# Kernel optimization log

Measured on AMD Instinct MI355X. Metric: run time of the kernel, lower is better.

The kernel has to match this reference:

```python
import jax, jax.numpy as jnp
import numpy as np

K = 16                 # k nearest neighbors
POS_LO, POS_HI = 0, 3  # position_slice
INF = jnp.float32(1e30)


def setup_inputs() -> dict:
    key = jax.random.key(0)
    k1, k2, k3 = jax.random.split(key, 3)
    B, N, F = 16, 2048, 128
    nodes = jax.random.normal(k1, (B, N, F), dtype=jnp.float32)
    T = jax.random.randint(k2, (B,), 0, 1024)
    taus = jax.random.randint(k3, (B,), 0, 1024)
    return {"nodes": nodes, "T": T, "taus": taus, "B": B}


def reference(nodes, T, taus, B):
    # Faithful, vectorized version of the per-batch causal KNN edge builder.
    # Original: for each batch b, sinks = pos[b, T[b]:T[b]+taus[b]],
    # sources = pos[b, :T[b]+taus[b]]; knn(source, sink, k) returns
    # (sink_local_idx, source_idx); keep edges where sink_local > source;
    # assemble COO adjacency (b, sink_local, source) with weight 1.
    # Here we return the equivalent DENSE [B, N, N] adjacency.
    pos = nodes[:, :, POS_LO:POS_HI]              # [B, N, d]
    N = pos.shape[1]
    i_idx = jnp.arange(N)                         # local sink index grid
    # global index of sink i in batch b is T[b] + i
    sink_gidx = jnp.clip(T[:, None] + i_idx[None, :], 0, N - 1)   # [B, N]
    sink_pos = jnp.take_along_axis(pos, sink_gidx[..., None], axis=1)  # [B, N, d]
    sink_valid = i_idx[None, :] < taus[:, None]                    # [B, N]
    src_valid = i_idx[None, :] < (T + taus)[:, None]               # [B, N]
    # squared distances sink->source: [B, N_sink, N_src]
    d2 = jnp.sum((sink_pos[:, :, None, :] - pos[:, None, :, :]) ** 2, axis=-1)
    d2 = jnp.where(src_valid[:, None, :], d2, INF)
    neg_vals, nbr = jax.lax.top_k(-d2, K)          # k smallest distances, [B, N, K]
    nbr_valid = neg_vals > -INF                    # source actually existed
    causal = i_idx[None, :, None] > nbr            # edge[0] > edge[1] mask (local sink idx)
    valid = sink_valid[:, :, None] & nbr_valid & causal
    adj = jnp.zeros((B, N, N), dtype=jnp.float32)
    b_idx = jnp.arange(B)[:, None, None]
    adj = adj.at[b_idx, i_idx[None, :, None], nbr].add(
        jnp.where(valid, jnp.float32(1.0), jnp.float32(0.0)))
    return adj
```

## Files before the change

kernel.cpp:

```cpp
#include <hip/hip_runtime.h>

#define NN 2048
#define FF 128
#define KK 16
#define INF_KEY 0xFFFFFFFFFFFFFFFFull

typedef float f32x4 __attribute__((ext_vector_type(4)));

__device__ __forceinline__ unsigned wave_min_u32(unsigned x) {
    int v = (int)x, t;
    t = __builtin_amdgcn_update_dpp(v, v, 0x111, 0xf, 0xf, false);
    v = ((unsigned)t < (unsigned)v) ? t : v;
    t = __builtin_amdgcn_update_dpp(v, v, 0x112, 0xf, 0xf, false);
    v = ((unsigned)t < (unsigned)v) ? t : v;
    t = __builtin_amdgcn_update_dpp(v, v, 0x114, 0xf, 0xf, false);
    v = ((unsigned)t < (unsigned)v) ? t : v;
    t = __builtin_amdgcn_update_dpp(v, v, 0x118, 0xf, 0xf, false);
    v = ((unsigned)t < (unsigned)v) ? t : v;
    t = __builtin_amdgcn_update_dpp(v, v, 0x142, 0xf, 0xf, false);
    v = ((unsigned)t < (unsigned)v) ? t : v;
    t = __builtin_amdgcn_update_dpp(v, v, 0x143, 0xf, 0xf, false);
    v = ((unsigned)t < (unsigned)v) ? t : v;
    return (unsigned)__builtin_amdgcn_readlane(v, 63);
}

__global__ __launch_bounds__(256) void pack_xyz(
    const float* __restrict__ nodes, f32x4* __restrict__ out, int total)
{
    const int t = blockIdx.x * 256 + threadIdx.x;
    if (t < total) {
        const float* p = nodes + (size_t)t * FF;
        out[t] = (f32x4){p[0], p[1], p[2], 0.f};
    }
}

template<bool PACKED>
__device__ __forceinline__ f32x4 load_xyz(const float* __restrict__ base, int idx) {
    if constexpr (PACKED) {
        return ((const f32x4*)base)[idx];
    } else {
        const float* p = base + (size_t)idx * FF;
        return (f32x4){p[0], p[1], p[2], 0.f};
    }
}

template<bool PACKED>
__global__ __launch_bounds__(256, 8) void knn_scatter(
    const float* __restrict__ xyz,
    const int*   __restrict__ T_arr,
    const int*   __restrict__ tau_arr,
    float*       __restrict__ adj)
{
    const int b    = blockIdx.x;
    const int i0   = blockIdx.y << 2;
    const int tid  = threadIdx.x;
    const int wave = tid >> 6;
    const int lane = tid & 63;

    const int tau = tau_arr[b];
    if (i0 >= tau) return;

    const int i = i0 + wave;
    if (i >= tau) return;

    const int T = T_arr[b];
    const int M = T + tau;
    const float* base = PACKED ? xyz + (size_t)b * NN * 4
                               : xyz + (size_t)b * NN * FF;
    float* row = adj + ((size_t)b * NN + i) * NN;

    const int g = T + i;
    const f32x4 sp = load_xyz<PACKED>(base, g);
    const float sxv = sp.x, syv = sp.y, szv = sp.z;

    unsigned long long q0 = INF_KEY, q1 = INF_KEY, q2 = INF_KEY, q3 = INF_KEY;
    const int S = (M + 63) >> 6;
    #pragma unroll 4
    for (int s = 0; s < S; ++s) {
        const int j = lane + (s << 6);
        if (j < M) {
            const f32x4 v = load_xyz<PACKED>(base, j);
            float dx = __fsub_rn(sxv, v.x);
            float dy = __fsub_rn(syv, v.y);
            float dz = __fsub_rn(szv, v.z);
            float d2 = __fadd_rn(__fadd_rn(__fmul_rn(dx, dx), __fmul_rn(dy, dy)),
                                 __fmul_rn(dz, dz));
            unsigned long long key =
                ((unsigned long long)__float_as_uint(d2) << 32) | (unsigned)(j + 1);
            if (key < q3) {
                q3 = key;
                unsigned long long t;
                if (q3 < q2) { t = q2; q2 = q3; q3 = t; }
                if (q2 < q1) { t = q1; q1 = q2; q2 = t; }
                if (q1 < q0) { t = q0; q0 = q1; q1 = t; }
            }
        }
    }

    unsigned long long lastpop = 0;
    for (int k = 0; k < KK; ++k) {
        const unsigned hd = (unsigned)(q0 >> 32);
        const unsigned m  = wave_min_u32(hd);
        if (m == 0xFFFFFFFFu) break;

        const unsigned long long mask = __ballot(hd == m);
        unsigned jwin;
        if (__popcll(mask) == 1) {
            const int w = __builtin_ctzll(mask);
            jwin = (unsigned)__builtin_amdgcn_readlane((int)(unsigned)q0, w);
        } else {
            unsigned jc = (hd == m) ? (unsigned)q0 : 0xFFFFFFFFu;
            jwin = wave_min_u32(jc);
        }
        const int j = (int)jwin - 1;

        if (lane == 0 && j < i)
            row[j] = 1.0f;

        if (hd == m && (unsigned)q0 == jwin) {
            lastpop = ((unsigned long long)m << 32) | jwin;
            q0 = q1; q1 = q2; q2 = q3; q3 = INF_KEY;
            if (q0 == INF_KEY) {
                unsigned long long best = INF_KEY;
                for (int s2 = 0; s2 < S; ++s2) {
                    const int jj = lane + (s2 << 6);
                    if (jj < M) {
                        const f32x4 v = load_xyz<PACKED>(base, jj);
                        float dx = __fsub_rn(sxv, v.x);
                        float dy = __fsub_rn(syv, v.y);
                        float dz = __fsub_rn(szv, v.z);
                        float d2 = __fadd_rn(
                            __fadd_rn(__fmul_rn(dx, dx), __fmul_rn(dy, dy)),
                            __fmul_rn(dz, dz));
                        unsigned long long kk =
                            ((unsigned long long)__float_as_uint(d2) << 32)
                            | (unsigned)(jj + 1);
                        if (kk > lastpop && kk < best) best = kk;
                    }
                }
                q0 = best;
            }
        }
    }
}

extern "C" void kernel_launch(void* const* d_in, const int* in_sizes, int n_in,
                              void* d_out, int out_size, void* d_ws, size_t ws_size,
                              hipStream_t stream) {
    const float* nodes = (const float*)d_in[0];
    const int*   T     = (const int*)d_in[1];
    const int*   taus  = (const int*)d_in[2];
    float*       adj   = (float*)d_out;
    const int B = in_sizes[1];

    const size_t out_bytes = (size_t)B * NN * NN * sizeof(float);
    hipMemsetAsync(adj, 0, out_bytes, stream);

    dim3 grid(B, 1024 / 4);
    const size_t need = (size_t)B * NN * sizeof(f32x4);
    if (d_ws != nullptr && ws_size >= need) {
        const int total = B * NN;
        pack_xyz<<<dim3((total + 255) / 256), dim3(256), 0, stream>>>(
            nodes, (f32x4*)d_ws, total);
        knn_scatter<true><<<grid, dim3(256), 0, stream>>>(
            (const float*)d_ws, T, taus, adj);
    } else {
        knn_scatter<false><<<grid, dim3(256), 0, stream>>>(
            nodes, T, taus, adj);
    }
}
```

Measured before the change: 312.4 us.

## Replace memset plus scatter with bitmask stage and dense nontemporal adjacency write

The KNN kernel now records selected neighbors as a per-row 2048-bit mask in workspace instead of scattering 1.0 values into a pre-zeroed output. A second kernel writes every adjacency row exactly once with vectorized nontemporal stores, expanding mask bits to floats, which removes the separate full-output memset pass. The xyz packing pre-pass is also dropped, so the KNN stage reads positions directly from the strided node array. This adds a small mask round trip and another launch.

```diff
diff --git a/kernel.cpp b/kernel.cpp
--- a/kernel.cpp
+++ b/kernel.cpp
@@ -3,6 +3,7 @@
 #define NN 2048
 #define FF 128
 #define KK 16
+#define MASKROWS 1024
 #define INF_KEY 0xFFFFFFFFFFFFFFFFull
 
 typedef float f32x4 __attribute__((ext_vector_type(4)));
@@ -24,38 +25,21 @@
     return (unsigned)__builtin_amdgcn_readlane(v, 63);
 }
 
-__global__ __launch_bounds__(256) void pack_xyz(
-    const float* __restrict__ nodes, f32x4* __restrict__ out, int total)
-{
-    const int t = blockIdx.x * 256 + threadIdx.x;
-    if (t < total) {
-        const float* p = nodes + (size_t)t * FF;
-        out[t] = (f32x4){p[0], p[1], p[2], 0.f};
-    }
-}
-
-template<bool PACKED>
-__device__ __forceinline__ f32x4 load_xyz(const float* __restrict__ base, int idx) {
-    if constexpr (PACKED) {
-        return ((const f32x4*)base)[idx];
-    } else {
-        const float* p = base + (size_t)idx * FF;
-        return (f32x4){p[0], p[1], p[2], 0.f};
-    }
-}
-
-template<bool PACKED>
-__global__ __launch_bounds__(256, 8) void knn_scatter(
-    const float* __restrict__ xyz,
+__device__ __forceinline__ f32x4 load_xyz(const float* __restrict__ nodes_b, int idx) {
+    const float* p = nodes_b + (size_t)idx * FF;
+    return (f32x4){p[0], p[1], p[2], 0.f};
+}
+
+__global__ __launch_bounds__(256, 8) void knn_mask(
+    const float* __restrict__ nodes,
     const int*   __restrict__ T_arr,
     const int*   __restrict__ tau_arr,
-    float*       __restrict__ adj)
+    unsigned*    __restrict__ mask)
 {
     const int b    = blockIdx.x;
     const int i0   = blockIdx.y << 2;
-    const int tid  = threadIdx.x;
-    const int wave = tid >> 6;
-    const int lane = tid & 63;
+    const int wave = threadIdx.x >> 6;
+    const int lane = threadIdx.x & 63;
 
     const int tau = tau_arr[b];
     if (i0 >= tau) return;
@@ -65,12 +49,10 @@
 
     const int T = T_arr[b];
     const int M = T + tau;
-    const float* base = PACKED ? xyz + (size_t)b * NN * 4
-                               : xyz + (size_t)b * NN * FF;
-    float* row = adj + ((size_t)b * NN + i) * NN;
+    const float* base = nodes + (size_t)b * NN * FF;
 
     const int g = T + i;
-    const f32x4 sp = load_xyz<PACKED>(base, g);
+    const f32x4 sp = load_xyz(base, g);
     const float sxv = sp.x, syv = sp.y, szv = sp.z;
 
     unsigned long long q0 = INF_KEY, q1 = INF_KEY, q2 = INF_KEY, q3 = INF_KEY;
@@ -79,7 +61,7 @@
     for (int s = 0; s < S; ++s) {
         const int j = lane + (s << 6);
         if (j < M) {
-            const f32x4 v = load_xyz<PACKED>(base, j);
+            const f32x4 v = load_xyz(base, j);
             float dx = __fsub_rn(sxv, v.x);
             float dy = __fsub_rn(syv, v.y);
             float dz = __fsub_rn(szv, v.z);
@@ -97,16 +79,17 @@
         }
     }
 
+    unsigned colmask = 0;
     unsigned long long lastpop = 0;
     for (int k = 0; k < KK; ++k) {
         const unsigned hd = (unsigned)(q0 >> 32);
         const unsigned m  = wave_min_u32(hd);
         if (m == 0xFFFFFFFFu) break;
 
-        const unsigned long long mask = __ballot(hd == m);
+        const unsigned long long bmask = __ballot(hd == m);
         unsigned jwin;
-        if (__popcll(mask) == 1) {
-            const int w = __builtin_ctzll(mask);
+        if (__popcll(bmask) == 1) {
+            const int w = __builtin_ctzll(bmask);
             jwin = (unsigned)__builtin_amdgcn_readlane((int)(unsigned)q0, w);
         } else {
             unsigned jc = (hd == m) ? (unsigned)q0 : 0xFFFFFFFFu;
@@ -114,8 +97,8 @@
         }
         const int j = (int)jwin - 1;
 
-        if (lane == 0 && j < i)
-            row[j] = 1.0f;
+        if (j < i && (j >> 5) == lane)
+            colmask |= 1u << (j & 31);
 
         if (hd == m && (unsigned)q0 == jwin) {
             lastpop = ((unsigned long long)m << 32) | jwin;
@@ -125,7 +108,7 @@
                 for (int s2 = 0; s2 < S; ++s2) {
                     const int jj = lane + (s2 << 6);
                     if (jj < M) {
-                        const f32x4 v = load_xyz<PACKED>(base, jj);
+                        const f32x4 v = load_xyz(base, jj);
                         float dx = __fsub_rn(sxv, v.x);
                         float dy = __fsub_rn(syv, v.y);
                         float dz = __fsub_rn(szv, v.z);
@@ -142,6 +125,140 @@
             }
         }
     }
+
+    mask[((size_t)(b * MASKROWS + i) << 6) + lane] = colmask;
+}
+
+__global__ __launch_bounds__(256) void write_adj(
+    const unsigned* __restrict__ mask,
+    const int*      __restrict__ tau_arr,
+    float*          __restrict__ adj)
+{
+    const int b    = blockIdx.x;
+    const int i0   = blockIdx.y << 2;
+    const int wave = threadIdx.x >> 6;
+    const int lane = threadIdx.x & 63;
+
+    const int tau = tau_arr[b];
+    const int i   = i0 + wave;
+    f32x4* out4 = (f32x4*)(adj + ((size_t)b * NN + i) * NN);
+
+    if (i >= tau) {
+        const f32x4 z = (f32x4){0.f, 0.f, 0.f, 0.f};
+        #pragma unroll
+        for (int k = 0; k < 8; ++k)
+            __builtin_nontemporal_store(z, &out4[(k << 6) + lane]);
+        return;
+    }
+
+    const unsigned* mrow = mask + ((size_t)(b * MASKROWS + i) << 6);
+    #pragma unroll
+    for (int k = 0; k < 8; ++k) {
+        const unsigned w   = mrow[(k << 3) + (lane >> 3)];
+        const unsigned nib = (w >> ((lane & 7) << 2)) & 0xFu;
+        f32x4 v;
+        v.x = (nib & 1u) ? 1.0f : 0.0f;
+        v.y = (nib & 2u) ? 1.0f : 0.0f;
+        v.z = (nib & 4u) ? 1.0f : 0.0f;
+        v.w = (nib & 8u) ? 1.0f : 0.0f;
+        __builtin_nontemporal_store(v, &out4[(k << 6) + lane]);
+    }
+}
+
+__global__ __launch_bounds__(256, 8) void knn_scatter_direct(
+    const float* __restrict__ nodes,
+    const int*   __restrict__ T_arr,
+    const int*   __restrict__ tau_arr,
+    float*       __restrict__ adj)
+{
+    const int b    = blockIdx.x;
+    const int i0   = blockIdx.y << 2;
+    const int wave = threadIdx.x >> 6;
+    const int lane = threadIdx.x & 63;
+
+    const int tau = tau_arr[b];
+    if (i0 >= tau) return;
+    const int i = i0 + wave;
+    if (i >= tau) return;
+
+    const int T = T_arr[b];
+    const int M = T + tau;
+    const float* base = nodes + (size_t)b * NN * FF;
+    float* row = adj + ((size_t)b * NN + i) * NN;
+
+    const int g = T + i;
+    const f32x4 sp = load_xyz(base, g);
+    const float sxv = sp.x, syv = sp.y, szv = sp.z;
+
+    unsigned long long q0 = INF_KEY, q1 = INF_KEY, q2 = INF_KEY, q3 = INF_KEY;
+    const int S = (M + 63) >> 6;
+    #pragma unroll 4
+    for (int s = 0; s < S; ++s) {
+        const int j = lane + (s << 6);
+        if (j < M) {
+            const f32x4 v = load_xyz(base, j);
+            float dx = __fsub_rn(sxv, v.x);
+            float dy = __fsub_rn(syv, v.y);
+            float dz = __fsub_rn(szv, v.z);
+            float d2 = __fadd_rn(__fadd_rn(__fmul_rn(dx, dx), __fmul_rn(dy, dy)),
+                                 __fmul_rn(dz, dz));
+            unsigned long long key =
+                ((unsigned long long)__float_as_uint(d2) << 32) | (unsigned)(j + 1);
+            if (key < q3) {
+                q3 = key;
+                unsigned long long t;
+                if (q3 < q2) { t = q2; q2 = q3; q3 = t; }
+                if (q2 < q1) { t = q1; q1 = q2; q2 = t; }
+                if (q1 < q0) { t = q0; q0 = q1; q1 = t; }
+            }
+        }
+    }
+
+    unsigned long long lastpop = 0;
+    for (int k = 0; k < KK; ++k) {
+        const unsigned hd = (unsigned)(q0 >> 32);
+        const unsigned m  = wave_min_u32(hd);
+        if (m == 0xFFFFFFFFu) break;
+
+        const unsigned long long bmask = __ballot(hd == m);
+        unsigned jwin;
+        if (__popcll(bmask) == 1) {
+            const int w = __builtin_ctzll(bmask);
+            jwin = (unsigned)__builtin_amdgcn_readlane((int)(unsigned)q0, w);
+        } else {
+            unsigned jc = (hd == m) ? (unsigned)q0 : 0xFFFFFFFFu;
+            jwin = wave_min_u32(jc);
+        }
+        const int j = (int)jwin - 1;
+
+        if (lane == 0 && j < i)
+            row[j] = 1.0f;
+
+        if (hd == m && (unsigned)q0 == jwin) {
+            lastpop = ((unsigned long long)m << 32) | jwin;
+            q0 = q1; q1 = q2; q2 = q3; q3 = INF_KEY;
+            if (q0 == INF_KEY) {
+                unsigned long long best = INF_KEY;
+                for (int s2 = 0; s2 < S; ++s2) {
+                    const int jj = lane + (s2 << 6);
+                    if (jj < M) {
+                        const f32x4 v = load_xyz(base, jj);
+                        float dx = __fsub_rn(sxv, v.x);
+                        float dy = __fsub_rn(syv, v.y);
+                        float dz = __fsub_rn(szv, v.z);
+                        float d2 = __fadd_rn(
+                            __fadd_rn(__fmul_rn(dx, dx), __fmul_rn(dy, dy)),
+                            __fmul_rn(dz, dz));
+                        unsigned long long kk =
+                            ((unsigned long long)__float_as_uint(d2) << 32)
+                            | (unsigned)(jj + 1);
+                        if (kk > lastpop && kk < best) best = kk;
+                    }
+                }
+                q0 = best;
+            }
+        }
+    }
 }
 
 extern "C" void kernel_launch(void* const* d_in, const int* in_sizes, int n_in,
@@ -153,19 +270,17 @@
     float*       adj   = (float*)d_out;
     const int B = in_sizes[1];
 
-    const size_t out_bytes = (size_t)B * NN * NN * sizeof(float);
-    hipMemsetAsync(adj, 0, out_bytes, stream);
-
-    dim3 grid(B, 1024 / 4);
-    const size_t need = (size_t)B * NN * sizeof(f32x4);
-    if (d_ws != nullptr && ws_size >= need) {
-        const int total = B * NN;
-        pack_xyz<<<dim3((total + 255) / 256), dim3(256), 0, stream>>>(
-            nodes, (f32x4*)d_ws, total);
-        knn_scatter<true><<<grid, dim3(256), 0, stream>>>(
-            (const float*)d_ws, T, taus, adj);
+    const size_t mask_bytes = (size_t)B * MASKROWS * 64 * sizeof(unsigned);
+
+    if (d_ws != nullptr && ws_size >= mask_bytes) {
+        knn_mask<<<dim3(B, MASKROWS / 4), dim3(256), 0, stream>>>(
+            nodes, T, taus, (unsigned*)d_ws);
+        write_adj<<<dim3(B, NN / 4), dim3(256), 0, stream>>>(
+            (const unsigned*)d_ws, taus, adj);
     } else {
-        knn_scatter<false><<<grid, dim3(256), 0, stream>>>(
+        const size_t out_bytes = (size_t)B * NN * NN * sizeof(float);
+        hipMemsetAsync(adj, 0, out_bytes, stream);
+        knn_scatter_direct<<<dim3(B, MASKROWS / 4), dim3(256), 0, stream>>>(
             nodes, T, taus, adj);
     }
 }
```

Result: slower. 337.4 us (+8.0%).
